# Optimization experiments

Measured on AMD Instinct MI355X. Metric: run time of the kernel, lower is better.

Reference implementation:

```python
import jax, jax.numpy as jnp
import numpy as np

NUM_HEADS = 16
EMBED_DIM = 1024

def setup_inputs() -> dict:
    key = jax.random.key(0)
    k1, k2, k3 = jax.random.split(key, 3)
    x = jax.random.normal(k1, (4, 2048, EMBED_DIM), dtype=jnp.float32)
    # Linear weights (lecun-style scaling for numerical sanity)
    w_qkv = jax.random.normal(k2, (EMBED_DIM, 3 * EMBED_DIM), dtype=jnp.float32) / np.sqrt(EMBED_DIM)
    w_out = jax.random.normal(k3, (EMBED_DIM, EMBED_DIM), dtype=jnp.float32) / np.sqrt(EMBED_DIM)
    return {"x": x, "w_qkv": w_qkv, "w_out": w_out}

def reference(x, w_qkv, w_out):
    b, s, d = x.shape
    h = NUM_HEADS
    dh = d // h
    qkv = x @ w_qkv                        # [b, s, 3d]
    q, k, v = jnp.split(qkv, 3, axis=-1)   # each [b, s, d]
    def split_heads(t):
        return t.reshape(b, s, h, dh).transpose(0, 2, 1, 3)  # [b, h, s, dh]
    q, k, v = split_heads(q), split_heads(k), split_heads(v)
    logits = jnp.einsum('bhsd,bhtd->bhst', q, k) / jnp.sqrt(jnp.asarray(dh, q.dtype))
    weights = jax.nn.softmax(logits, axis=-1)
    out = jnp.einsum('bhst,bhtd->bhsd', weights, v)
    out = out.transpose(0, 2, 1, 3).reshape(b, s, d)  # [b, s, d]
    return out @ w_out
```

## Files before the change

kernel.cpp:

```cpp
#include <hip/hip_runtime.h>
#include <hip/hip_bf16.h>
#include <math.h>

typedef unsigned short u16;
typedef unsigned long long u64;
typedef __attribute__((ext_vector_type(8))) short short8;
typedef __attribute__((ext_vector_type(4))) float floatx4;

#define BB 4
#define SS 2048
#define DD 1024
#define HH 16
#define DHH 64
#define BSZ (BB*SS)

__device__ inline u16 bf1(float f) {
  return (u16)((__float_as_uint(f) + 0x8000u) >> 16);
}
__device__ inline unsigned pk2bf(float a, float b) {
  return __builtin_amdgcn_perm(__float_as_uint(b) + 0x8000u,
                               __float_as_uint(a) + 0x8000u, 0x07060302u);
}
__device__ inline unsigned pkbf(float a, float b) {
  unsigned r;
  asm("v_cvt_pk_bf16_f32 %0, %1, %2" : "=v"(r) : "v"(a), "v"(b));
  return r;
}

__device__ inline short8 ld16(const u16* p) {
  union { uint4 u; short8 s; } cv;
  cv.u = *(const uint4*)p;
  return cv.s;
}

__device__ inline void gload_lds16(const u16* g, u16* l) {
  __builtin_amdgcn_global_load_lds(
      (const __attribute__((address_space(1))) void*)g,
      (__attribute__((address_space(3))) void*)l, 16, 0, 0);
}

__device__ inline void swap_qpair(unsigned &a, unsigned &b) {
  asm("v_permlane32_swap_b32 %0, %1" : "+v"(a), "+v"(b));
  asm("v_permlane16_swap_b32 %0, %1" : "+v"(a), "+v"(b));
}

__global__ __launch_bounds__(256) void cvt_f32_bf16(
    const float* __restrict__ in, u16* __restrict__ out) {
  int t = blockIdx.x * 256 + threadIdx.x;
  const float4* p = (const float4*)in + (size_t)t * 2;
  float4 a = p[0], b = p[1];
  uint4 r;
  r.x = pk2bf(a.x, a.y); r.y = pk2bf(a.z, a.w);
  r.z = pk2bf(b.x, b.y); r.w = pk2bf(b.z, b.w);
  *((uint4*)out + t) = r;
}

__global__ __launch_bounds__(256) void transpose_f32_bf16(
    const float* __restrict__ in, u16* __restrict__ out, int K, int N) {
  __shared__ u16 tile[32][33];
  int k0 = blockIdx.y * 32, n0 = blockIdx.x * 32;
  int tx = threadIdx.x, ty = threadIdx.y;
  #pragma unroll
  for (int i = 0; i < 32; i += 8)
    tile[ty + i][tx] = bf1(in[(size_t)(k0 + ty + i) * N + n0 + tx]);
  __syncthreads();
  #pragma unroll
  for (int i = 0; i < 32; i += 8)
    out[(size_t)(n0 + ty + i) * K + k0 + tx] = tile[tx][ty + i];
}

template <int MODE>
__global__ __launch_bounds__(256) void gemm_nt(
    const u16* __restrict__ A, const u16* __restrict__ Bt,
    int M, int N, int K,
    float* __restrict__ outf, u16* __restrict__ q, u16* __restrict__ kk,
    u16* __restrict__ vv) {
  __shared__ __attribute__((aligned(16))) u16 As[128 * 32];
  __shared__ __attribute__((aligned(16))) u16 Bs[128 * 32];
  const int tid = threadIdx.x;
  const int lane = tid & 63;
  const int wave = tid >> 6;
  const int col = lane & 15, quad = lane >> 4;
  const int nbx = gridDim.x;
  const int nwg = nbx * gridDim.y;
  const int lin = blockIdx.y * nbx + blockIdx.x;
  const int swz = (lin & 7) * (nwg >> 3) + (lin >> 3);
  const int m0 = (swz / nbx) * 128, n0 = (swz % nbx) * 128;
  const int wm = (wave & 1) * 64, wn = (wave >> 1) * 64;

  floatx4 acc[4][4];
  #pragma unroll
  for (int i = 0; i < 4; i++)
    #pragma unroll
    for (int j = 0; j < 4; j++) acc[i][j] = (floatx4){0.f, 0.f, 0.f, 0.f};

  const u16* ga0 = A + (size_t)(m0 + (tid >> 2)) * K + (tid & 3) * 8;
  const u16* ga1 = ga0 + (size_t)64 * K;
  const u16* gb0 = Bt + (size_t)(n0 + (tid >> 2)) * K + (tid & 3) * 8;
  const u16* gb1 = gb0 + (size_t)64 * K;
  u16* lA0 = As + wave * 512;
  u16* lB0 = Bs + wave * 512;

  for (int kb = 0; kb < K; kb += 32) {
    __syncthreads();
    gload_lds16(ga0 + kb, lA0);
    gload_lds16(ga1 + kb, lA0 + 2048);
    gload_lds16(gb0 + kb, lB0);
    gload_lds16(gb1 + kb, lB0 + 2048);
    __syncthreads();
    short8 af[4], bfr[4];
    #pragma unroll
    for (int i = 0; i < 4; i++)
      af[i] = ld16(As + (wm + i * 16 + col) * 32 + quad * 8);
    #pragma unroll
    for (int i = 0; i < 4; i++)
      bfr[i] = ld16(Bs + (wn + i * 16 + col) * 32 + quad * 8);
    #pragma unroll
    for (int i = 0; i < 4; i++)
      #pragma unroll
      for (int j = 0; j < 4; j++)
        acc[i][j] = __builtin_amdgcn_mfma_f32_16x16x32_bf16(af[i], bfr[j],
                                                            acc[i][j], 0, 0, 0);
  }

  #pragma unroll
  for (int i = 0; i < 4; i++) {
    #pragma unroll
    for (int j = 0; j < 4; j++) {
      int gm0 = m0 + wm + i * 16 + quad * 4;
      int gn = n0 + wn + j * 16 + col;
      if (MODE == 0) {
        #pragma unroll
        for (int r = 0; r < 4; r++)
          outf[(size_t)(gm0 + r) * N + gn] = acc[i][j][r];
      } else {
        int which = gn >> 10;
        if (which == 2) {
          int dh = gn & 63, hh = (gn >> 6) & 15;
          int bb = gm0 >> 11, s = gm0 & 2047;
          uint2 pk;
          pk.x = pk2bf(acc[i][j][0], acc[i][j][1]);
          pk.y = pk2bf(acc[i][j][2], acc[i][j][3]);
          *(uint2*)(vv + ((size_t)((bb * HH + hh) * 64 + dh)) * SS + s) = pk;
        } else {
          int f = gn & 1023;
          u16* dst = (which == 0) ? q : kk;
          float sc = (which == 0) ? 0.18033688f : 1.0f;
          #pragma unroll
          for (int r = 0; r < 4; r++)
            dst[(size_t)(gm0 + r) * DD + f] = bf1(acc[i][j][r] * sc);
        }
      }
    }
  }
}

__global__ __launch_bounds__(256, 2) void attn_kernel(
    const u16* __restrict__ Q, const u16* __restrict__ K,
    const u16* __restrict__ VT, u16* __restrict__ O) {
  __shared__ __attribute__((aligned(16))) u16 Ks[64 * 72];
  __shared__ __attribute__((aligned(16))) u16 Vs[64 * 72];

  const int tid = threadIdx.x, lane = tid & 63, wave = tid >> 6;
  const int col = lane & 15, quad = lane >> 4;
  const int bid = blockIdx.x;
  const int idx = ((bid & 7) << 6) + (bid >> 3);
  const int qt = idx & 7;
  const int h = (idx >> 3) & 15;
  const int b = idx >> 7;

  const size_t rowbase = (size_t)b * SS;
  const int qrow0 = qt * 256 + wave * 64;

  short8 qf[4][2];
  #pragma unroll
  for (int qs = 0; qs < 4; qs++)
    #pragma unroll
    for (int kc = 0; kc < 2; kc++)
      qf[qs][kc] = ld16(Q + (rowbase + qrow0 + qs * 16 + col) * DD + h * DHH +
                        kc * 32 + quad * 8);

  const u16* kg = K + rowbase * DD + h * DHH;
  const u16* vg = VT + (size_t)(b * HH + h) * DHH * SS;

  union { unsigned u[4]; short8 s8; } onesf;
  {
    unsigned ow = (col == 0) ? 0x3F803F80u : 0u;
    onesf.u[0] = ow; onesf.u[1] = ow; onesf.u[2] = ow; onesf.u[3] = ow;
  }

  floatx4 o[4][5];
  #pragma unroll
  for (int qs = 0; qs < 4; qs++)
    #pragma unroll
    for (int mt = 0; mt < 5; mt++) o[qs][mt] = (floatx4){0.f, 0.f, 0.f, 0.f};

  const int srow = tid >> 2, sc = (tid & 3) * 16;

  uint4 k0 = *(const uint4*)(kg + (size_t)srow * DD + sc);
  uint4 k1 = *(const uint4*)(kg + (size_t)srow * DD + sc + 8);
  uint4 v0 = *(const uint4*)(vg + (size_t)srow * SS + sc);
  uint4 v1 = *(const uint4*)(vg + (size_t)srow * SS + sc + 8);

  for (int kt = 0; kt < SS; kt += 64) {
    __syncthreads();
    *(uint4*)(Ks + srow * 72 + sc) = k0;
    *(uint4*)(Ks + srow * 72 + sc + 8) = k1;
    *(uint4*)(Vs + srow * 72 + sc) = v0;
    *(uint4*)(Vs + srow * 72 + sc + 8) = v1;
    __syncthreads();

    if (kt + 64 < SS) {
      k0 = *(const uint4*)(kg + (size_t)(kt + 64 + srow) * DD + sc);
      k1 = *(const uint4*)(kg + (size_t)(kt + 64 + srow) * DD + sc + 8);
      v0 = *(const uint4*)(vg + (size_t)srow * SS + kt + 64 + sc);
      v1 = *(const uint4*)(vg + (size_t)srow * SS + kt + 64 + sc + 8);
    }

    #pragma unroll
    for (int h2 = 0; h2 < 2; h2++) {
      unsigned pk[4][2][2];
      #pragma unroll
      for (int mtl = 0; mtl < 2; mtl++) {
        const int mt = h2 * 2 + mtl;
        short8 kf0 = ld16(Ks + (mt * 16 + col) * 72 + quad * 8);
        short8 kf1 = ld16(Ks + (mt * 16 + col) * 72 + 32 + quad * 8);
        #pragma unroll
        for (int qs = 0; qs < 4; qs++) {
          floatx4 s = (floatx4){0.f, 0.f, 0.f, 0.f};
          __builtin_amdgcn_s_setprio(1);
          s = __builtin_amdgcn_mfma_f32_16x16x32_bf16(kf0, qf[qs][0], s, 0, 0, 0);
          s = __builtin_amdgcn_mfma_f32_16x16x32_bf16(kf1, qf[qs][1], s, 0, 0, 0);
          __builtin_amdgcn_s_setprio(0);
          pk[qs][mtl][0] =
              pkbf(__builtin_amdgcn_exp2f(s[0]), __builtin_amdgcn_exp2f(s[1]));
          pk[qs][mtl][1] =
              pkbf(__builtin_amdgcn_exp2f(s[2]), __builtin_amdgcn_exp2f(s[3]));
        }
      }
      short8 va[4];
      #pragma unroll
      for (int mt5 = 0; mt5 < 4; mt5++)
        va[mt5] = ld16(Vs + (mt5 * 16 + col) * 72 + h2 * 32 + quad * 8);
      #pragma unroll
      for (int qs = 0; qs < 4; qs++) {
        unsigned wa = pk[qs][0][0], wb = pk[qs][1][0];
        swap_qpair(wa, wb);
        unsigned wc = pk[qs][0][1], wd = pk[qs][1][1];
        swap_qpair(wc, wd);
        union { unsigned u[4]; short8 s8; } bb;
        bb.u[0] = wa; bb.u[1] = wc; bb.u[2] = wb; bb.u[3] = wd;
        __builtin_amdgcn_s_setprio(1);
        #pragma unroll
        for (int mt5 = 0; mt5 < 4; mt5++)
          o[qs][mt5] = __builtin_amdgcn_mfma_f32_16x16x32_bf16(
              va[mt5], bb.s8, o[qs][mt5], 0, 0, 0);
        o[qs][4] = __builtin_amdgcn_mfma_f32_16x16x32_bf16(
            onesf.s8, bb.s8, o[qs][4], 0, 0, 0);
        __builtin_amdgcn_s_setprio(0);
      }
    }
  }

  #pragma unroll
  for (int qs = 0; qs < 4; qs++) {
    float l = __shfl(o[qs][4][0], col, 64);
    float inv = 1.0f / l;
    u16* ob = O + (rowbase + qrow0 + qs * 16 + col) * DD + h * DHH;
    #pragma unroll
    for (int mt = 0; mt < 4; mt++) {
      uint2 pk;
      pk.x = pkbf(o[qs][mt][0] * inv, o[qs][mt][1] * inv);
      pk.y = pkbf(o[qs][mt][2] * inv, o[qs][mt][3] * inv);
      *(uint2*)(ob + mt * 16 + quad * 4) = pk;
    }
  }
}

extern "C" void kernel_launch(void* const* d_in, const int* in_sizes, int n_in,
                              void* d_out, int out_size, void* d_ws,
                              size_t ws_size, hipStream_t stream) {
  const float* x = (const float*)d_in[0];
  const float* w_qkv = (const float*)d_in[1];
  const float* w_out = (const float*)d_in[2];
  float* out = (float*)d_out;

  u16* ws = (u16*)d_ws;
  u16* wT = ws;
  u16* q = wT + (size_t)3072 * 1024;
  u16* vt = q + (size_t)BSZ * DD;
  u16* k = (u16*)d_out;
  u16* xb = k + (size_t)BSZ * DD;
  u16* att = q;

  cvt_f32_bf16<<<dim3(BSZ * DD / (256 * 8)), 256, 0, stream>>>(x, xb);
  transpose_f32_bf16<<<dim3(3072 / 32, 1024 / 32), dim3(32, 8), 0, stream>>>(
      w_qkv, wT, 1024, 3072);
  gemm_nt<1><<<dim3(3072 / 128, BSZ / 128), 256, 0, stream>>>(
      xb, wT, BSZ, 3072, 1024, nullptr, q, k, vt);
  transpose_f32_bf16<<<dim3(1024 / 32, 1024 / 32), dim3(32, 8), 0, stream>>>(
      w_out, wT, 1024, 1024);
  attn_kernel<<<dim3(BB * HH * (SS / 256)), 256, 0, stream>>>(q, k, vt, att);
  gemm_nt<0><<<dim3(1024 / 128, BSZ / 128), 256, 0, stream>>>(
      att, wT, BSZ, 1024, 1024, out, nullptr, nullptr, nullptr);
}
```

Measured before the change: 270.5 us.

## Replace QKV projection GEMM with 256x256-tile 8-wave pipelined kernel

Adds a new QKV projection GEMM using 256x256 output tiles with 512 threads (8 waves, each computing a 128x64 subtile), a 128KB double-buffered LDS staged via global_load_lds, and interleaved prefetch with explicit vmcnt waits and s_setprio around MFMA bursts. The goal is more data reuse per LDS load and overlap of global loads with MFMA work, replacing the older 128x128 kernel. The larger tile yields only 384 workgroups and uses 128KB of LDS, so occupancy is lower, and the epilogue still uses scattered 2-byte stores for Q/K.

```diff
diff --git a/kernel.cpp b/kernel.cpp
--- a/kernel.cpp
+++ b/kernel.cpp
@@ -43,6 +43,8 @@
   asm("v_permlane32_swap_b32 %0, %1" : "+v"(a), "+v"(b));
   asm("v_permlane16_swap_b32 %0, %1" : "+v"(a), "+v"(b));
 }
+
+#define VMCNT(n) asm volatile("s_waitcnt vmcnt(" #n ")" ::: "memory")
 
 __global__ __launch_bounds__(256) void cvt_f32_bf16(
     const float* __restrict__ in, u16* __restrict__ out) {
@@ -67,6 +69,136 @@
   #pragma unroll
   for (int i = 0; i < 32; i += 8)
     out[(size_t)(n0 + ty + i) * K + k0 + tx] = tile[tx][ty + i];
+}
+
+__global__ __launch_bounds__(512, 2) void gemm8p_nt(
+    const u16* __restrict__ A, const u16* __restrict__ Bt, int K,
+    u16* __restrict__ q, u16* __restrict__ kk, u16* __restrict__ vv) {
+  __shared__ __attribute__((aligned(16))) u16 sh[65536];
+  const int tid = threadIdx.x;
+  const int lane = tid & 63, wave = tid >> 6;
+  const int col = lane & 15, quad = lane >> 4;
+  const int wm = (wave >> 2) * 128;
+  const int wn = (wave & 3) * 64;
+  const int nbx = gridDim.x;
+  const int nwg = nbx * gridDim.y;
+  const int lin = blockIdx.y * nbx + blockIdx.x;
+  const int swz = (lin & 7) * (nwg >> 3) + (lin >> 3);
+  const int m0 = (swz / nbx) * 256, n0 = (swz % nbx) * 256;
+
+  floatx4 acc[8][4];
+  #pragma unroll
+  for (int i = 0; i < 8; i++)
+    #pragma unroll
+    for (int j = 0; j < 4; j++) acc[i][j] = (floatx4){0.f, 0.f, 0.f, 0.f};
+
+  const int srow = tid & 255, sg = tid >> 8;
+  const u16* ga = A + (size_t)(m0 + srow) * K + sg * 8;
+  const u16* gb = Bt + (size_t)(n0 + srow) * K + sg * 8;
+  u16* lw = sh + wave * 512;
+
+  #define STG(mat, gbase, db, ks, tk) do {                                   \
+    gload_lds16(gbase + (tk)*64 + (ks)*32,                                   \
+                lw + (db)*32768 + (mat)*16384 + (ks)*8192);                  \
+    gload_lds16(gbase + (tk)*64 + (ks)*32 + 16,                              \
+                lw + (db)*32768 + (mat)*16384 + (ks)*8192 + 4096);           \
+  } while (0)
+
+  const int NT = K >> 6;
+  STG(0, ga, 0, 0, 0);
+  STG(1, gb, 0, 0, 0);
+  STG(0, ga, 0, 1, 0);
+  STG(1, gb, 0, 1, 0);
+
+  for (int tk = 0; tk < NT; ++tk) {
+    const int db = tk & 1;
+    const u16* Ab = sh + db * 32768;
+    const u16* Bb = sh + db * 32768 + 16384;
+    const bool more = (tk + 1) < NT;
+    short8 af[8], b0, b1;
+
+    VMCNT(4);
+    __builtin_amdgcn_s_barrier();
+    __builtin_amdgcn_sched_barrier(0);
+    if (more) STG(0, ga, db ^ 1, 0, tk + 1);
+    #pragma unroll
+    for (int mf = 0; mf < 8; mf++)
+      af[mf] = ld16(Ab + quad * 2048 + (wm + mf * 16 + col) * 8);
+    b0 = ld16(Bb + quad * 2048 + (wn + col) * 8);
+    b1 = ld16(Bb + quad * 2048 + (wn + 16 + col) * 8);
+    __builtin_amdgcn_s_setprio(1);
+    #pragma unroll
+    for (int mf = 0; mf < 8; mf++) {
+      acc[mf][0] = __builtin_amdgcn_mfma_f32_16x16x32_bf16(af[mf], b0, acc[mf][0], 0, 0, 0);
+      acc[mf][1] = __builtin_amdgcn_mfma_f32_16x16x32_bf16(af[mf], b1, acc[mf][1], 0, 0, 0);
+    }
+    __builtin_amdgcn_s_setprio(0);
+
+    if (more) STG(1, gb, db ^ 1, 0, tk + 1);
+    b0 = ld16(Bb + quad * 2048 + (wn + 32 + col) * 8);
+    b1 = ld16(Bb + quad * 2048 + (wn + 48 + col) * 8);
+    __builtin_amdgcn_s_setprio(1);
+    #pragma unroll
+    for (int mf = 0; mf < 8; mf++) {
+      acc[mf][2] = __builtin_amdgcn_mfma_f32_16x16x32_bf16(af[mf], b0, acc[mf][2], 0, 0, 0);
+      acc[mf][3] = __builtin_amdgcn_mfma_f32_16x16x32_bf16(af[mf], b1, acc[mf][3], 0, 0, 0);
+    }
+    __builtin_amdgcn_s_setprio(0);
+
+    if (tk == NT - 1) { VMCNT(0); } else { VMCNT(4); }
+    __builtin_amdgcn_s_barrier();
+    __builtin_amdgcn_sched_barrier(0);
+    if (more) STG(0, ga, db ^ 1, 1, tk + 1);
+    #pragma unroll
+    for (int mf = 0; mf < 8; mf++)
+      af[mf] = ld16(Ab + 8192 + quad * 2048 + (wm + mf * 16 + col) * 8);
+    b0 = ld16(Bb + 8192 + quad * 2048 + (wn + col) * 8);
+    b1 = ld16(Bb + 8192 + quad * 2048 + (wn + 16 + col) * 8);
+    __builtin_amdgcn_s_setprio(1);
+    #pragma unroll
+    for (int mf = 0; mf < 8; mf++) {
+      acc[mf][0] = __builtin_amdgcn_mfma_f32_16x16x32_bf16(af[mf], b0, acc[mf][0], 0, 0, 0);
+      acc[mf][1] = __builtin_amdgcn_mfma_f32_16x16x32_bf16(af[mf], b1, acc[mf][1], 0, 0, 0);
+    }
+    __builtin_amdgcn_s_setprio(0);
+
+    if (more) STG(1, gb, db ^ 1, 1, tk + 1);
+    b0 = ld16(Bb + 8192 + quad * 2048 + (wn + 32 + col) * 8);
+    b1 = ld16(Bb + 8192 + quad * 2048 + (wn + 48 + col) * 8);
+    __builtin_amdgcn_s_setprio(1);
+    #pragma unroll
+    for (int mf = 0; mf < 8; mf++) {
+      acc[mf][2] = __builtin_amdgcn_mfma_f32_16x16x32_bf16(af[mf], b0, acc[mf][2], 0, 0, 0);
+      acc[mf][3] = __builtin_amdgcn_mfma_f32_16x16x32_bf16(af[mf], b1, acc[mf][3], 0, 0, 0);
+    }
+    __builtin_amdgcn_s_setprio(0);
+  }
+  #undef STG
+
+  #pragma unroll
+  for (int mf = 0; mf < 8; mf++) {
+    #pragma unroll
+    for (int nf = 0; nf < 4; nf++) {
+      int gm0 = m0 + wm + mf * 16 + quad * 4;
+      int gn = n0 + wn + nf * 16 + col;
+      int which = gn >> 10;
+      if (which == 2) {
+        int dh = gn & 63, hh = (gn >> 6) & 15;
+        int bb2 = gm0 >> 11, s = gm0 & 2047;
+        uint2 pk;
+        pk.x = pk2bf(acc[mf][nf][0], acc[mf][nf][1]);
+        pk.y = pk2bf(acc[mf][nf][2], acc[mf][nf][3]);
+        *(uint2*)(vv + ((size_t)((bb2 * HH + hh) * 64 + dh)) * SS + s) = pk;
+      } else {
+        int f = gn & 1023;
+        u16* dst = (which == 0) ? q : kk;
+        float sc = (which == 0) ? 0.18033688f : 1.0f;
+        #pragma unroll
+        for (int r = 0; r < 4; r++)
+          dst[(size_t)(gm0 + r) * DD + f] = bf1(acc[mf][nf][r] * sc);
+      }
+    }
+  }
 }
 
 template <int MODE>
@@ -296,8 +428,8 @@
   cvt_f32_bf16<<<dim3(BSZ * DD / (256 * 8)), 256, 0, stream>>>(x, xb);
   transpose_f32_bf16<<<dim3(3072 / 32, 1024 / 32), dim3(32, 8), 0, stream>>>(
       w_qkv, wT, 1024, 3072);
-  gemm_nt<1><<<dim3(3072 / 128, BSZ / 128), 256, 0, stream>>>(
-      xb, wT, BSZ, 3072, 1024, nullptr, q, k, vt);
+  gemm8p_nt<<<dim3(3072 / 256, BSZ / 256), 512, 0, stream>>>(
+      xb, wT, 1024, q, k, vt);
   transpose_f32_bf16<<<dim3(1024 / 32, 1024 / 32), dim3(32, 8), 0, stream>>>(
       w_out, wT, 1024, 1024);
   attn_kernel<<<dim3(BB * HH * (SS / 256)), 256, 0, stream>>>(q, k, vt, att);
```

New measurement: 301.3 us. 11.4% more time.

## Double GEMM K-tile to 64 with k-major LDS layout and fuse prep kernels

Applied to the files above, without the earlier changes.

The GEMM main loop now stages a 64-wide K slice per iteration instead of 32. Each row is loaded as four 16-element k-chunks into a k-chunk-major LDS layout, which halves the number of barrier pairs per GEMM and changes the LDS read pattern for the MFMA fragments. Separately, the x fp32-to-bf16 conversion and the w_qkv transpose are merged into one launch that dispatches on block index, saving a kernel launch. The cost is doubled LDS use per block, which may reduce occupancy, and a different bank-access pattern.

```diff
diff --git a/kernel.cpp b/kernel.cpp
--- a/kernel.cpp
+++ b/kernel.cpp
@@ -44,15 +44,32 @@
   asm("v_permlane16_swap_b32 %0, %1" : "+v"(a), "+v"(b));
 }
 
-__global__ __launch_bounds__(256) void cvt_f32_bf16(
-    const float* __restrict__ in, u16* __restrict__ out) {
-  int t = blockIdx.x * 256 + threadIdx.x;
-  const float4* p = (const float4*)in + (size_t)t * 2;
-  float4 a = p[0], b = p[1];
-  uint4 r;
-  r.x = pk2bf(a.x, a.y); r.y = pk2bf(a.z, a.w);
-  r.z = pk2bf(b.x, b.y); r.w = pk2bf(b.z, b.w);
-  *((uint4*)out + t) = r;
+__global__ __launch_bounds__(256) void prep_kernel(
+    const float* __restrict__ x, u16* __restrict__ xb,
+    const float* __restrict__ w_qkv, u16* __restrict__ wT) {
+  __shared__ u16 tile[32][33];
+  const int bid = blockIdx.x, tid = threadIdx.x;
+  if (bid < 4096) {
+    int t = bid * 256 + tid;
+    const float4* p = (const float4*)x + (size_t)t * 2;
+    float4 a = p[0], b = p[1];
+    uint4 r;
+    r.x = pk2bf(a.x, a.y); r.y = pk2bf(a.z, a.w);
+    r.z = pk2bf(b.x, b.y); r.w = pk2bf(b.z, b.w);
+    *((uint4*)xb + t) = r;
+  } else {
+    const int local = bid - 4096;
+    const int K = 1024, N = 3072;
+    int n0 = (local % 96) * 32, k0 = (local / 96) * 32;
+    int tx = tid & 31, ty = tid >> 5;
+    #pragma unroll
+    for (int i = 0; i < 32; i += 8)
+      tile[ty + i][tx] = bf1(w_qkv[(size_t)(k0 + ty + i) * N + n0 + tx]);
+    __syncthreads();
+    #pragma unroll
+    for (int i = 0; i < 32; i += 8)
+      wT[(size_t)(n0 + ty + i) * K + k0 + tx] = tile[tx][ty + i];
+  }
 }
 
 __global__ __launch_bounds__(256) void transpose_f32_bf16(
@@ -75,8 +92,8 @@
     int M, int N, int K,
     float* __restrict__ outf, u16* __restrict__ q, u16* __restrict__ kk,
     u16* __restrict__ vv) {
-  __shared__ __attribute__((aligned(16))) u16 As[128 * 32];
-  __shared__ __attribute__((aligned(16))) u16 Bs[128 * 32];
+  __shared__ __attribute__((aligned(16))) u16 As[128 * 64];
+  __shared__ __attribute__((aligned(16))) u16 Bs[128 * 64];
   const int tid = threadIdx.x;
   const int lane = tid & 63;
   const int wave = tid >> 6;
@@ -94,33 +111,36 @@
     #pragma unroll
     for (int j = 0; j < 4; j++) acc[i][j] = (floatx4){0.f, 0.f, 0.f, 0.f};
 
-  const u16* ga0 = A + (size_t)(m0 + (tid >> 2)) * K + (tid & 3) * 8;
-  const u16* ga1 = ga0 + (size_t)64 * K;
-  const u16* gb0 = Bt + (size_t)(n0 + (tid >> 2)) * K + (tid & 3) * 8;
-  const u16* gb1 = gb0 + (size_t)64 * K;
-  u16* lA0 = As + wave * 512;
-  u16* lB0 = Bs + wave * 512;
-
-  for (int kb = 0; kb < K; kb += 32) {
-    __syncthreads();
-    gload_lds16(ga0 + kb, lA0);
-    gload_lds16(ga1 + kb, lA0 + 2048);
-    gload_lds16(gb0 + kb, lB0);
-    gload_lds16(gb1 + kb, lB0 + 2048);
-    __syncthreads();
-    short8 af[4], bfr[4];
-    #pragma unroll
-    for (int i = 0; i < 4; i++)
-      af[i] = ld16(As + (wm + i * 16 + col) * 32 + quad * 8);
-    #pragma unroll
-    for (int i = 0; i < 4; i++)
-      bfr[i] = ld16(Bs + (wn + i * 16 + col) * 32 + quad * 8);
-    #pragma unroll
-    for (int i = 0; i < 4; i++)
+  const int sr = tid & 127, sg = tid >> 7;
+  const u16* gaS = A + (size_t)(m0 + sr) * K + sg * 8;
+  const u16* gbS = Bt + (size_t)(n0 + sr) * K + sg * 8;
+  u16* lA = As + wave * 512;
+  u16* lB = Bs + wave * 512;
+
+  for (int kb = 0; kb < K; kb += 64) {
+    __syncthreads();
+    #pragma unroll
+    for (int j2 = 0; j2 < 4; j2++) {
+      gload_lds16(gaS + kb + j2 * 16, lA + j2 * 2048);
+      gload_lds16(gbS + kb + j2 * 16, lB + j2 * 2048);
+    }
+    __syncthreads();
+    #pragma unroll
+    for (int kc = 0; kc < 2; kc++) {
+      short8 af[4], bfr[4];
+      #pragma unroll
+      for (int i = 0; i < 4; i++)
+        af[i] = ld16(As + (kc * 4 + quad) * 1024 + (wm + i * 16 + col) * 8);
       #pragma unroll
       for (int j = 0; j < 4; j++)
-        acc[i][j] = __builtin_amdgcn_mfma_f32_16x16x32_bf16(af[i], bfr[j],
-                                                            acc[i][j], 0, 0, 0);
+        bfr[j] = ld16(Bs + (kc * 4 + quad) * 1024 + (wn + j * 16 + col) * 8);
+      #pragma unroll
+      for (int i = 0; i < 4; i++)
+        #pragma unroll
+        for (int j = 0; j < 4; j++)
+          acc[i][j] = __builtin_amdgcn_mfma_f32_16x16x32_bf16(af[i], bfr[j],
+                                                              acc[i][j], 0, 0, 0);
+    }
   }
 
   #pragma unroll
@@ -293,9 +313,7 @@
   u16* xb = k + (size_t)BSZ * DD;
   u16* att = q;
 
-  cvt_f32_bf16<<<dim3(BSZ * DD / (256 * 8)), 256, 0, stream>>>(x, xb);
-  transpose_f32_bf16<<<dim3(3072 / 32, 1024 / 32), dim3(32, 8), 0, stream>>>(
-      w_qkv, wT, 1024, 3072);
+  prep_kernel<<<dim3(4096 + 3072), 256, 0, stream>>>(x, xb, w_qkv, wT);
   gemm_nt<1><<<dim3(3072 / 128, BSZ / 128), 256, 0, stream>>>(
       xb, wT, BSZ, 3072, 1024, nullptr, q, k, vt);
   transpose_f32_bf16<<<dim3(1024 / 32, 1024 / 32), dim3(32, 8), 0, stream>>>(
```

Result: slower. 323.0 us (+19.4%).
